# Kernel tuning notes

Measured on AMD Instinct MI355X. Metric: run time of the kernel, lower is better.

## Reference

```python
import jax, jax.numpy as jnp
import numpy as np

E = 400000   # n_entity
R = 500      # n_relation
D = 128      # embed_dim
B = 2048     # batch of queries
K = 128      # sample_limit (refer neighbors per query)
GAMMA = 24.0
EPS = 2.0


def _xavier(key, fan_out, fan_in):
    lim = np.sqrt(6.0 / (fan_in + fan_out)).astype(np.float32)
    return jax.random.uniform(key, (fan_out, fan_in), minval=-lim, maxval=lim, dtype=jnp.float32)


def setup_inputs() -> dict:
    key = jax.random.key(0)
    ks = jax.random.split(key, 9)
    erange = (GAMMA + EPS) / D
    # tables with the appended zero padding row (as in forward's torch.cat)
    ent = jax.random.uniform(ks[0], (E + R + 1, D), minval=-erange, maxval=erange, dtype=jnp.float32)
    entity_embedding = jnp.concatenate([ent, jnp.zeros((1, D), jnp.float32)], axis=0)
    rel = jax.random.uniform(ks[1], (R + 1, D), minval=-erange, maxval=erange, dtype=jnp.float32)
    relation_embedding = jnp.concatenate([rel, jnp.zeros((1, D), jnp.float32)], axis=0)
    off = jax.random.uniform(ks[2], (R + 1, D), minval=0.0, maxval=erange, dtype=jnp.float32)
    offset_embedding = jnp.concatenate([off, jnp.zeros((1, D), jnp.float32)], axis=0)
    # ProjectionAggregating attention MLP params
    W1 = _xavier(ks[3], D, 2 * D)
    b1 = jnp.zeros((D,), jnp.float32)
    W2 = _xavier(ks[4], D, D)
    b2 = jnp.zeros((D,), jnp.float32)
    anchors = jax.random.randint(ks[5], (B,), 0, E)
    rel_0 = jax.random.randint(ks[6], (B,), 0, R)
    p1_target = jax.random.randint(ks[7], (B, K), 0, E)
    p1_rel = jax.random.randint(ks[8], (B, K), 0, R)
    return {
        'entity_embedding': entity_embedding,
        'relation_embedding': relation_embedding,
        'offset_embedding': offset_embedding,
        'W1': W1, 'b1': b1, 'W2': W2, 'b2': b2,
        'anchors': anchors, 'rel_0': rel_0,
        'p1_target': p1_target, 'p1_rel': p1_rel,
    }


def reference(entity_embedding, relation_embedding, offset_embedding,
              W1, b1, W2, b2, anchors, rel_0, p1_target, p1_rel):
    # ---- '1p' query path of IDN_Q2B_24.forward ----
    h_a = entity_embedding[anchors]            # [B, D]
    r_q = relation_embedding[rel_0]            # [B, D]
    query_emb = h_a + r_q                      # [B, D]
    offset_emb = offset_embedding[rel_0]       # [B, D]  (activation = Identity)
    h_t = entity_embedding[p1_target]          # [B, K, D]  refer_embs
    r_t = relation_embedding[p1_rel]           # [B, K, D]  refer_r
    # ProjectionAggregating (aggr='bias'): bias = refer - (start + refer_r)
    bias = h_t - (h_a[:, None, :] + r_t)       # [B, K, D]
    x = jnp.concatenate([r_t, jnp.broadcast_to(r_q[:, None, :], r_t.shape)], axis=-1)  # [B,K,2D]
    a1 = jax.nn.relu(jnp.einsum('bkf,df->bkd', x, W1) + b1)   # [B, K, D]
    attn = jnp.einsum('bkd,ed->bke', a1, W2) + b2             # [B, K, D]
    final_refer = jnp.sum(attn * bias, axis=-2)               # [B, D]
    final_query = query_emb + final_refer
    return final_query, offset_emb
```

## Files before the change

### kernel.cpp

```cpp
#include <hip/hip_runtime.h>

typedef __attribute__((ext_vector_type(8))) short short8;
typedef __attribute__((ext_vector_type(4))) float f32x4;

#define NRELROWS 502
#define NB 2048
#define DD 128
#define OUT_HALF (NB * DD)
#define NPRE 158

__device__ __forceinline__ short f2bf(float x) {
    union { float f; unsigned u; } c; c.f = x;
    return (short)((c.u + 0x7FFFu + ((c.u >> 16) & 1u)) >> 16);
}

__global__ __launch_bounds__(256) void precompute_kernel(
    const float* __restrict__ rel, const float* __restrict__ W1,
    const float* __restrict__ b1, const float* __restrict__ W2,
    float* __restrict__ U, float* __restrict__ V,
    unsigned short* __restrict__ W2f, float* __restrict__ out)
{
    const int bid = blockIdx.x;
    const int tid = threadIdx.x;
    for (int i = bid * 256 + tid; i < OUT_HALF; i += NPRE * 256)
        out[i] = 0.f;

    if (bid < 126) {
        __shared__ float srel[4][DD];
        const int r0 = bid << 2;
        for (int i = tid; i < 512; i += 256) {
            const int r = i >> 7, c = i & 127;
            const int rr = r0 + r;
            srel[r][c] = (rr < NRELROWS) ? rel[rr * DD + c] : 0.f;
        }
        __syncthreads();
        const int half = tid >> 7;
        const int d = tid & 127;
        const float* wrow = W1 + d * 256 + half * 128;
        float a0 = 0.f, a1 = 0.f, a2 = 0.f, a3 = 0.f;
#pragma unroll 8
        for (int f = 0; f < 128; f += 4) {
            const float4 wv = *(const float4*)(wrow + f);
            a0 += srel[0][f]*wv.x + srel[0][f+1]*wv.y + srel[0][f+2]*wv.z + srel[0][f+3]*wv.w;
            a1 += srel[1][f]*wv.x + srel[1][f+1]*wv.y + srel[1][f+2]*wv.z + srel[1][f+3]*wv.w;
            a2 += srel[2][f]*wv.x + srel[2][f+1]*wv.y + srel[2][f+2]*wv.z + srel[2][f+3]*wv.w;
            a3 += srel[3][f]*wv.x + srel[3][f+1]*wv.y + srel[3][f+2]*wv.z + srel[3][f+3]*wv.w;
        }
        float res[4] = {a0, a1, a2, a3};
        const float bb = half ? b1[d] : 0.f;
#pragma unroll
        for (int r = 0; r < 4; ++r) {
            if (r0 + r < NRELROWS) {
                if (half) V[(r0 + r) * DD + d] = res[r] + bb;
                else      U[(r0 + r) * DD + d] = res[r];
            }
        }
    } else if (bid < NPRE) {
        const int tile = bid - 126;
        const int kt = tile >> 3, nt = tile & 7;
#pragma unroll
        for (int e = 0; e < 2; ++e) {
            const int within = tid * 2 + e;
            const int ll = within >> 3, ii = within & 7;
            const int n = nt * 16 + (ll & 15);
            const int f = kt * 32 + (ll >> 4) * 8 + ii;
            W2f[tile * 512 + within] = (unsigned short)f2bf(W2[n * 128 + f]);
        }
    }
}

__global__ __launch_bounds__(256, 2) void main_kernel(
    const float* __restrict__ ent, const float* __restrict__ rel,
    const float* __restrict__ off, const float* __restrict__ b2,
    const int* __restrict__ anchors, const int* __restrict__ rel0,
    const int* __restrict__ p1t, const int* __restrict__ p1r,
    const float* __restrict__ U, const float* __restrict__ V,
    const unsigned short* __restrict__ W2f, float* __restrict__ out)
{
    __shared__ float ht[64][DD];
    __shared__ unsigned short w2l[32 * 512];
    const int bid = blockIdx.x;
    const int b  = bid >> 1;
    const int kh = bid & 1;
    const int tid = threadIdx.x;
    const int w = tid >> 6;
    const int l = tid & 63;
    const int lg = l >> 4;
    const int l15 = l & 15;
    const int hlf = l >> 5;

    const int* p1t_b = p1t + (b << 7) + (kh << 6);
    const int* p1r_b = p1r + (b << 7) + (kh << 6);

#pragma unroll
    for (int i = 0; i < 8; ++i) {
        const int chunk = (w << 3) + i;
        const unsigned short* g = W2f + chunk * 512 + (l << 3);
        unsigned short* lp = w2l + chunk * 512;
        __builtin_amdgcn_global_load_lds(
            (const __attribute__((address_space(1))) unsigned int*)g,
            (__attribute__((address_space(3))) unsigned int*)lp, 16, 0, 0);
    }
    __builtin_amdgcn_sched_barrier(0);

    const int aidx = anchors[b];
    const int r0 = rel0[b];
    int rowi[8];
#pragma unroll
    for (int j = 0; j < 8; ++j)
        rowi[j] = p1t_b[(w << 4) + (j << 1) + hlf];
    const int relA = p1r_b[(w << 4) + l15];
    const int4 rr4 = *(const int4*)(p1r_b + (w << 4) + (lg << 2));
    __builtin_amdgcn_sched_barrier(0);

    const float* Vrow = V + r0 * DD;
    const float* Urow = U + relA * DD;
    float4 u0[4], u1[4], v0[4], v1[4];
#pragma unroll
    for (int kt = 0; kt < 4; ++kt) {
        const int f0 = kt * 32 + lg * 8;
        u0[kt] = *(const float4*)(Urow + f0);
        u1[kt] = *(const float4*)(Urow + f0 + 4);
        v0[kt] = *(const float4*)(Vrow + f0);
        v1[kt] = *(const float4*)(Vrow + f0 + 4);
    }
    const int rrk[4] = {rr4.x, rr4.y, rr4.z, rr4.w};
    float rv[4][8], hav[8], b2v[8];
#pragma unroll
    for (int r2 = 0; r2 < 4; ++r2) {
        const float* rp = rel + rrk[r2] * DD + l15;
#pragma unroll
        for (int nt = 0; nt < 8; ++nt) rv[r2][nt] = rp[nt << 4];
    }
    const float* ar = ent + (size_t)aidx * DD + l15;
#pragma unroll
    for (int nt = 0; nt < 8; ++nt) {
        hav[nt] = ar[nt << 4];
        b2v[nt] = b2[(nt << 4) + l15];
    }
    float o_a = 0.f, o_r = 0.f, o_o = 0.f;
    if (kh == 0 && tid < DD) {
        o_a = ent[(size_t)aidx * DD + tid];
        o_r = rel[r0 * DD + tid];
        o_o = off[r0 * DD + tid];
    }
    __builtin_amdgcn_sched_barrier(0);

#pragma unroll
    for (int j = 0; j < 8; ++j) {
        const float* g = ent + (size_t)rowi[j] * DD + ((l & 31) << 2);
        float* lp = &ht[(w << 4) + (j << 1)][0];
        __builtin_amdgcn_global_load_lds(
            (const __attribute__((address_space(1))) unsigned int*)g,
            (__attribute__((address_space(3))) unsigned int*)lp, 16, 0, 0);
    }
    __builtin_amdgcn_sched_barrier(0);

    short8 af[4];
#pragma unroll
    for (int kt = 0; kt < 4; ++kt) {
        af[kt][0] = f2bf(fmaxf(u0[kt].x + v0[kt].x, 0.f));
        af[kt][1] = f2bf(fmaxf(u0[kt].y + v0[kt].y, 0.f));
        af[kt][2] = f2bf(fmaxf(u0[kt].z + v0[kt].z, 0.f));
        af[kt][3] = f2bf(fmaxf(u0[kt].w + v0[kt].w, 0.f));
        af[kt][4] = f2bf(fmaxf(u1[kt].x + v1[kt].x, 0.f));
        af[kt][5] = f2bf(fmaxf(u1[kt].y + v1[kt].y, 0.f));
        af[kt][6] = f2bf(fmaxf(u1[kt].z + v1[kt].z, 0.f));
        af[kt][7] = f2bf(fmaxf(u1[kt].w + v1[kt].w, 0.f));
    }

    __builtin_amdgcn_s_barrier();

    f32x4 acc[8];
#pragma unroll
    for (int nt = 0; nt < 8; ++nt) acc[nt] = (f32x4)0.f;
#pragma unroll
    for (int kt = 0; kt < 4; ++kt) {
#pragma unroll
        for (int nt = 0; nt < 8; ++nt) {
            const short8 bf = *(const short8*)(w2l + ((kt << 3) + nt) * 512 + (l << 3));
            acc[nt] = __builtin_amdgcn_mfma_f32_16x16x32_bf16(af[kt], bf, acc[nt], 0, 0, 0);
        }
    }

    asm volatile("s_waitcnt vmcnt(0)" ::: "memory");
    __builtin_amdgcn_sched_barrier(0);

    float psv[8];
#pragma unroll
    for (int nt = 0; nt < 8; ++nt) {
        const int d = (nt << 4) + l15;
        float p = 0.f;
#pragma unroll
        for (int r2 = 0; r2 < 4; ++r2) {
            const float at = acc[nt][r2] + b2v[nt];
            const float hv = ht[(w << 4) + (lg << 2) + r2][d];
            p += at * (hv - hav[nt] - rv[r2][nt]);
        }
        p += __shfl_xor(p, 16);
        p += __shfl_xor(p, 32);
        psv[nt] = p;
    }

    __syncthreads();
    float* red = &ht[0][0];
    if (lg == 0) {
#pragma unroll
        for (int nt = 0; nt < 8; ++nt)
            red[w * DD + (nt << 4) + l15] = psv[nt];
    }
    __syncthreads();
    if (tid < DD) {
        const float s = red[tid] + red[DD + tid] + red[2 * DD + tid] + red[3 * DD + tid];
        if (kh == 0) {
            atomicAdd(out + (b << 7) + tid, o_a + o_r + s);
            out[OUT_HALF + (b << 7) + tid] = o_o;
        } else {
            atomicAdd(out + (b << 7) + tid, s);
        }
    }
}

extern "C" void kernel_launch(void* const* d_in, const int* in_sizes, int n_in,
                              void* d_out, int out_size, void* d_ws, size_t ws_size,
                              hipStream_t stream) {
    const float* ent  = (const float*)d_in[0];
    const float* rel  = (const float*)d_in[1];
    const float* off  = (const float*)d_in[2];
    const float* W1   = (const float*)d_in[3];
    const float* b1   = (const float*)d_in[4];
    const float* W2   = (const float*)d_in[5];
    const float* b2   = (const float*)d_in[6];
    const int* anchors = (const int*)d_in[7];
    const int* rel0    = (const int*)d_in[8];
    const int* p1t     = (const int*)d_in[9];
    const int* p1r     = (const int*)d_in[10];
    float* out = (float*)d_out;

    float* U = (float*)d_ws;
    float* V = U + NRELROWS * DD;
    unsigned short* W2f = (unsigned short*)(V + NRELROWS * DD);

    precompute_kernel<<<NPRE, 256, 0, stream>>>(rel, W1, b1, W2, U, V, W2f, out);
    main_kernel<<<NB * 2, 256, 0, stream>>>(ent, rel, off, b2, anchors, rel0,
                                            p1t, p1r, U, V, W2f, out);
}
```

Baseline: 59.06 us.

## Assign one wave per query with double-buffered neighbor tiles and drop atomics

The main kernel is restructured so that each wave owns a whole query. A wave loops over eight 16-neighbor tiles and double-buffers the gathered entity rows in LDS, prefetching the next tile's indices, U rows and entity rows while the current tile's MFMA and reduction run. Because each query now has a single writer, the atomicAdd across K-halves, the cross-wave LDS reduction and the output zeroing in the precompute kernel all go away. The cost is a large dynamic LDS allocation that allows only one 512-thread block per CU, and 256 blocks in total, which reduces the parallelism available to hide gather latency.

```diff
diff --git a/kernel.cpp b/kernel.cpp
--- a/kernel.cpp
+++ b/kernel.cpp
@@ -7,7 +7,6 @@
 #define NB 2048
 #define DD 128
 #define OUT_HALF (NB * DD)
-#define NPRE 158
 
 __device__ __forceinline__ short f2bf(float x) {
     union { float f; unsigned u; } c; c.f = x;
@@ -18,13 +17,10 @@
     const float* __restrict__ rel, const float* __restrict__ W1,
     const float* __restrict__ b1, const float* __restrict__ W2,
     float* __restrict__ U, float* __restrict__ V,
-    unsigned short* __restrict__ W2f, float* __restrict__ out)
+    unsigned short* __restrict__ W2f)
 {
     const int bid = blockIdx.x;
     const int tid = threadIdx.x;
-    for (int i = bid * 256 + tid; i < OUT_HALF; i += NPRE * 256)
-        out[i] = 0.f;
-
     if (bid < 126) {
         __shared__ float srel[4][DD];
         const int r0 = bid << 2;
@@ -55,7 +51,7 @@
                 else      U[(r0 + r) * DD + d] = res[r];
             }
         }
-    } else if (bid < NPRE) {
+    } else {
         const int tile = bid - 126;
         const int kt = tile >> 3, nt = tile & 7;
 #pragma unroll
@@ -69,7 +65,7 @@
     }
 }
 
-__global__ __launch_bounds__(256, 2) void main_kernel(
+__global__ __launch_bounds__(512, 2) void main_kernel(
     const float* __restrict__ ent, const float* __restrict__ rel,
     const float* __restrict__ off, const float* __restrict__ b2,
     const int* __restrict__ anchors, const int* __restrict__ rel0,
@@ -77,24 +73,22 @@
     const float* __restrict__ U, const float* __restrict__ V,
     const unsigned short* __restrict__ W2f, float* __restrict__ out)
 {
-    __shared__ float ht[64][DD];
-    __shared__ unsigned short w2l[32 * 512];
-    const int bid = blockIdx.x;
-    const int b  = bid >> 1;
-    const int kh = bid & 1;
+    extern __shared__ char ldsraw[];
     const int tid = threadIdx.x;
-    const int w = tid >> 6;
-    const int l = tid & 63;
-    const int lg = l >> 4;
-    const int l15 = l & 15;
-    const int hlf = l >> 5;
-
-    const int* p1t_b = p1t + (b << 7) + (kh << 6);
-    const int* p1r_b = p1r + (b << 7) + (kh << 6);
-
-#pragma unroll
-    for (int i = 0; i < 8; ++i) {
-        const int chunk = (w << 3) + i;
+    const int w  = __builtin_amdgcn_readfirstlane(tid >> 6);
+    const int l  = tid & 63;
+    const int lg = l >> 4, l15 = l & 15, hlf = l >> 5;
+    unsigned short* w2l = (unsigned short*)(ldsraw + 131072);
+    float* hb0 = (float*)(ldsraw + w * 16384);
+    float* hb1 = (float*)(ldsraw + w * 16384 + 8192);
+
+    const int q = (blockIdx.x << 3) + w;
+    const int* p1t_q = p1t + (q << 7);
+    const int* p1r_q = p1r + (q << 7);
+
+#pragma unroll
+    for (int i = 0; i < 4; ++i) {
+        const int chunk = (w << 2) + i;
         const unsigned short* g = W2f + chunk * 512 + (l << 3);
         unsigned short* lp = w2l + chunk * 512;
         __builtin_amdgcn_global_load_lds(
@@ -103,121 +97,182 @@
     }
     __builtin_amdgcn_sched_barrier(0);
 
-    const int aidx = anchors[b];
-    const int r0 = rel0[b];
-    int rowi[8];
-#pragma unroll
-    for (int j = 0; j < 8; ++j)
-        rowi[j] = p1t_b[(w << 4) + (j << 1) + hlf];
-    const int relA = p1r_b[(w << 4) + l15];
-    const int4 rr4 = *(const int4*)(p1r_b + (w << 4) + (lg << 2));
-    __builtin_amdgcn_sched_barrier(0);
-
+    const int aidx = anchors[q];
+    const int r0 = rel0[q];
+    int relA = p1r_q[l15];
+    int4 rr4 = *(const int4*)(p1r_q + (lg << 2));
+    int rowi0[8];
+#pragma unroll
+    for (int j = 0; j < 8; ++j) rowi0[j] = p1t_q[(j << 1) + hlf];
+    __builtin_amdgcn_sched_barrier(0);
+
+    float4 v0[4], v1[4], nu0[4], nu1[4];
     const float* Vrow = V + r0 * DD;
     const float* Urow = U + relA * DD;
-    float4 u0[4], u1[4], v0[4], v1[4];
 #pragma unroll
     for (int kt = 0; kt < 4; ++kt) {
         const int f0 = kt * 32 + lg * 8;
-        u0[kt] = *(const float4*)(Urow + f0);
-        u1[kt] = *(const float4*)(Urow + f0 + 4);
         v0[kt] = *(const float4*)(Vrow + f0);
         v1[kt] = *(const float4*)(Vrow + f0 + 4);
-    }
-    const int rrk[4] = {rr4.x, rr4.y, rr4.z, rr4.w};
-    float rv[4][8], hav[8], b2v[8];
-#pragma unroll
-    for (int r2 = 0; r2 < 4; ++r2) {
-        const float* rp = rel + rrk[r2] * DD + l15;
-#pragma unroll
-        for (int nt = 0; nt < 8; ++nt) rv[r2][nt] = rp[nt << 4];
-    }
+        nu0[kt] = *(const float4*)(Urow + f0);
+        nu1[kt] = *(const float4*)(Urow + f0 + 4);
+    }
+    float b2v[8], hav[8];
     const float* ar = ent + (size_t)aidx * DD + l15;
 #pragma unroll
     for (int nt = 0; nt < 8; ++nt) {
+        b2v[nt] = b2[(nt << 4) + l15];
         hav[nt] = ar[nt << 4];
-        b2v[nt] = b2[(nt << 4) + l15];
-    }
-    float o_a = 0.f, o_r = 0.f, o_o = 0.f;
-    if (kh == 0 && tid < DD) {
-        o_a = ent[(size_t)aidx * DD + tid];
-        o_r = rel[r0 * DD + tid];
-        o_o = off[r0 * DD + tid];
     }
     __builtin_amdgcn_sched_barrier(0);
 
 #pragma unroll
     for (int j = 0; j < 8; ++j) {
-        const float* g = ent + (size_t)rowi[j] * DD + ((l & 31) << 2);
-        float* lp = &ht[(w << 4) + (j << 1)][0];
+        const float* g = ent + (size_t)rowi0[j] * DD + ((l & 31) << 2);
+        float* lp = hb0 + (j << 1) * DD;
         __builtin_amdgcn_global_load_lds(
             (const __attribute__((address_space(1))) unsigned int*)g,
             (__attribute__((address_space(3))) unsigned int*)lp, 16, 0, 0);
     }
     __builtin_amdgcn_sched_barrier(0);
 
+    asm volatile("s_waitcnt vmcnt(8)" ::: "memory");
+    __builtin_amdgcn_sched_barrier(0);
     short8 af[4];
 #pragma unroll
     for (int kt = 0; kt < 4; ++kt) {
-        af[kt][0] = f2bf(fmaxf(u0[kt].x + v0[kt].x, 0.f));
-        af[kt][1] = f2bf(fmaxf(u0[kt].y + v0[kt].y, 0.f));
-        af[kt][2] = f2bf(fmaxf(u0[kt].z + v0[kt].z, 0.f));
-        af[kt][3] = f2bf(fmaxf(u0[kt].w + v0[kt].w, 0.f));
-        af[kt][4] = f2bf(fmaxf(u1[kt].x + v1[kt].x, 0.f));
-        af[kt][5] = f2bf(fmaxf(u1[kt].y + v1[kt].y, 0.f));
-        af[kt][6] = f2bf(fmaxf(u1[kt].z + v1[kt].z, 0.f));
-        af[kt][7] = f2bf(fmaxf(u1[kt].w + v1[kt].w, 0.f));
-    }
-
+        af[kt][0] = f2bf(fmaxf(nu0[kt].x + v0[kt].x, 0.f));
+        af[kt][1] = f2bf(fmaxf(nu0[kt].y + v0[kt].y, 0.f));
+        af[kt][2] = f2bf(fmaxf(nu0[kt].z + v0[kt].z, 0.f));
+        af[kt][3] = f2bf(fmaxf(nu0[kt].w + v0[kt].w, 0.f));
+        af[kt][4] = f2bf(fmaxf(nu1[kt].x + v1[kt].x, 0.f));
+        af[kt][5] = f2bf(fmaxf(nu1[kt].y + v1[kt].y, 0.f));
+        af[kt][6] = f2bf(fmaxf(nu1[kt].z + v1[kt].z, 0.f));
+        af[kt][7] = f2bf(fmaxf(nu1[kt].w + v1[kt].w, 0.f));
+    }
     __builtin_amdgcn_s_barrier();
 
-    f32x4 acc[8];
-#pragma unroll
-    for (int nt = 0; nt < 8; ++nt) acc[nt] = (f32x4)0.f;
-#pragma unroll
-    for (int kt = 0; kt < 4; ++kt) {
+    float ps[8];
+#pragma unroll
+    for (int nt = 0; nt < 8; ++nt) ps[nt] = 0.f;
+
+#pragma unroll 1
+    for (int t = 0; t < 8; ++t) {
+        const int last = (t == 7);
+        float* hbr = (t & 1) ? hb1 : hb0;
+        float* hbw = (t & 1) ? hb0 : hb1;
+
+        f32x4 acc[8];
+#pragma unroll
+        for (int nt = 0; nt < 8; ++nt) acc[nt] = (f32x4)0.f;
+#pragma unroll
+        for (int kt = 0; kt < 4; ++kt) {
+#pragma unroll
+            for (int nt = 0; nt < 8; ++nt) {
+                const short8 bf = *(const short8*)(w2l + ((kt << 3) + nt) * 512 + (l << 3));
+                acc[nt] = __builtin_amdgcn_mfma_f32_16x16x32_bf16(af[kt], bf, acc[nt], 0, 0, 0);
+            }
+        }
+        __builtin_amdgcn_sched_barrier(0);
+
+        int relA_n = 0;
+        int4 rr4_n = {0, 0, 0, 0};
+        int rowi_n[8];
+        if (!last) {
+            const int tb = (t + 1) << 4;
+            relA_n = p1r_q[tb + l15];
+            rr4_n = *(const int4*)(p1r_q + tb + (lg << 2));
+#pragma unroll
+            for (int j = 0; j < 8; ++j) rowi_n[j] = p1t_q[tb + (j << 1) + hlf];
+        }
+        __builtin_amdgcn_sched_barrier(0);
+
+        if (!last) {
+            const float* Un = U + relA_n * DD;
+#pragma unroll
+            for (int kt = 0; kt < 4; ++kt) {
+                const int f0 = kt * 32 + lg * 8;
+                nu0[kt] = *(const float4*)(Un + f0);
+                nu1[kt] = *(const float4*)(Un + f0 + 4);
+            }
+        }
+        float rv[4][8];
+        {
+            const int rrk[4] = {rr4.x, rr4.y, rr4.z, rr4.w};
+#pragma unroll
+            for (int r2 = 0; r2 < 4; ++r2) {
+                const float* rp = rel + rrk[r2] * DD + l15;
+#pragma unroll
+                for (int nt = 0; nt < 8; ++nt) rv[r2][nt] = rp[nt << 4];
+            }
+        }
+        __builtin_amdgcn_sched_barrier(0);
+
+        if (!last) {
+#pragma unroll
+            for (int j = 0; j < 8; ++j) {
+                const float* g = ent + (size_t)rowi_n[j] * DD + ((l & 31) << 2);
+                float* lp = hbw + (j << 1) * DD;
+                __builtin_amdgcn_global_load_lds(
+                    (const __attribute__((address_space(1))) unsigned int*)g,
+                    (__attribute__((address_space(3))) unsigned int*)lp, 16, 0, 0);
+            }
+        }
+        __builtin_amdgcn_sched_barrier(0);
+
+        if (!last) asm volatile("s_waitcnt vmcnt(8)" ::: "memory");
+        else       asm volatile("s_waitcnt vmcnt(0)" ::: "memory");
+        __builtin_amdgcn_sched_barrier(0);
 #pragma unroll
         for (int nt = 0; nt < 8; ++nt) {
-            const short8 bf = *(const short8*)(w2l + ((kt << 3) + nt) * 512 + (l << 3));
-            acc[nt] = __builtin_amdgcn_mfma_f32_16x16x32_bf16(af[kt], bf, acc[nt], 0, 0, 0);
-        }
-    }
-
-    asm volatile("s_waitcnt vmcnt(0)" ::: "memory");
-    __builtin_amdgcn_sched_barrier(0);
-
-    float psv[8];
+            const int d = (nt << 4) + l15;
+#pragma unroll
+            for (int r2 = 0; r2 < 4; ++r2) {
+                const float at = acc[nt][r2] + b2v[nt];
+                const float hv = hbr[((lg << 2) + r2) * DD + d];
+                ps[nt] += at * (hv - hav[nt] - rv[r2][nt]);
+            }
+        }
+
+        if (!last) {
+#pragma unroll
+            for (int kt = 0; kt < 4; ++kt) {
+                af[kt][0] = f2bf(fmaxf(nu0[kt].x + v0[kt].x, 0.f));
+                af[kt][1] = f2bf(fmaxf(nu0[kt].y + v0[kt].y, 0.f));
+                af[kt][2] = f2bf(fmaxf(nu0[kt].z + v0[kt].z, 0.f));
+                af[kt][3] = f2bf(fmaxf(nu0[kt].w + v0[kt].w, 0.f));
+                af[kt][4] = f2bf(fmaxf(nu1[kt].x + v1[kt].x, 0.f));
+                af[kt][5] = f2bf(fmaxf(nu1[kt].y + v1[kt].y, 0.f));
+                af[kt][6] = f2bf(fmaxf(nu1[kt].z + v1[kt].z, 0.f));
+                af[kt][7] = f2bf(fmaxf(nu1[kt].w + v1[kt].w, 0.f));
+            }
+            relA = relA_n;
+            rr4 = rr4_n;
+        }
+    }
+
 #pragma unroll
     for (int nt = 0; nt < 8; ++nt) {
-        const int d = (nt << 4) + l15;
-        float p = 0.f;
-#pragma unroll
-        for (int r2 = 0; r2 < 4; ++r2) {
-            const float at = acc[nt][r2] + b2v[nt];
-            const float hv = ht[(w << 4) + (lg << 2) + r2][d];
-            p += at * (hv - hav[nt] - rv[r2][nt]);
-        }
-        p += __shfl_xor(p, 16);
-        p += __shfl_xor(p, 32);
-        psv[nt] = p;
-    }
-
-    __syncthreads();
-    float* red = &ht[0][0];
+        ps[nt] += __shfl_xor(ps[nt], 16);
+        ps[nt] += __shfl_xor(ps[nt], 32);
+    }
+    float orrv[8], offv[8];
+    const float* rr0p = rel + r0 * DD + l15;
+    const float* ofp  = off + r0 * DD + l15;
+#pragma unroll
+    for (int nt = 0; nt < 8; ++nt) {
+        orrv[nt] = rr0p[nt << 4];
+        offv[nt] = ofp[nt << 4];
+    }
     if (lg == 0) {
 #pragma unroll
         for (int nt = 0; nt < 8; ++nt)
-            red[w * DD + (nt << 4) + l15] = psv[nt];
-    }
-    __syncthreads();
-    if (tid < DD) {
-        const float s = red[tid] + red[DD + tid] + red[2 * DD + tid] + red[3 * DD + tid];
-        if (kh == 0) {
-            atomicAdd(out + (b << 7) + tid, o_a + o_r + s);
-            out[OUT_HALF + (b << 7) + tid] = o_o;
-        } else {
-            atomicAdd(out + (b << 7) + tid, s);
-        }
+            out[(q << 7) + (nt << 4) + l15] = hav[nt] + orrv[nt] + ps[nt];
+    }
+    if (lg == 1) {
+#pragma unroll
+        for (int nt = 0; nt < 8; ++nt)
+            out[OUT_HALF + (q << 7) + (nt << 4) + l15] = offv[nt];
     }
 }
 
@@ -241,7 +296,11 @@
     float* V = U + NRELROWS * DD;
     unsigned short* W2f = (unsigned short*)(V + NRELROWS * DD);
 
-    precompute_kernel<<<NPRE, 256, 0, stream>>>(rel, W1, b1, W2, U, V, W2f, out);
-    main_kernel<<<NB * 2, 256, 0, stream>>>(ent, rel, off, b2, anchors, rel0,
-                                            p1t, p1r, U, V, W2f, out);
+    const int lds_bytes = 8 * 16384 + 32 * 512 * 2;
+    hipFuncSetAttribute((const void*)main_kernel,
+                        hipFuncAttributeMaxDynamicSharedMemorySize, lds_bytes);
+
+    precompute_kernel<<<126 + 32, 256, 0, stream>>>(rel, W1, b1, W2, U, V, W2f);
+    main_kernel<<<NB / 8, 512, lds_bytes, stream>>>(ent, rel, off, b2, anchors, rel0,
+                                                    p1t, p1r, U, V, W2f, out);
 }
```

Result: slower. 61.79 us (+4.6%).
